# Kernel optimization log

Hardware: AMD Instinct MI355X
Metric: run time of the kernel (lower is better)

## Reference

```python
import jax, jax.numpy as jnp
import numpy as np

B, T, C, H, U = 16, 2048, 512, 4, 250
L, R = 1, 1              # l_order, r_order -> depthwise kernel size 3
K = L + R + 1
SMOOTH, NOISE = 1.0, 0.0  # smooth_factor, noise_threshold


def setup_inputs() -> dict:
    key = jax.random.key(0)
    k0, k1, k2, k3 = jax.random.split(key, 4)
    hidden = jax.random.normal(k0, (B, T, C), dtype=jnp.float32)
    mask = jnp.ones((B, 1, T), dtype=jnp.float32)
    target_label_length = jax.random.randint(k1, (B,), 0, U).astype(jnp.int32)
    # parameters
    conv_w = jax.random.normal(k2, (C, 1, K), dtype=jnp.float32) / np.sqrt(K)   # depthwise Conv1d weight [O, I/g=1, K]
    conv_b = jnp.zeros((C,), dtype=jnp.float32)
    lin_w = jax.random.normal(k3, (1, C), dtype=jnp.float32) / np.sqrt(C)       # cif_output Linear(idim, 1)
    lin_b = jnp.zeros((1,), dtype=jnp.float32)
    sigma = jnp.full((H,), 0.5, dtype=jnp.float32)
    sigma_bias = jnp.zeros((H,), dtype=jnp.float32)
    return {
        "hidden": hidden, "mask": mask, "target_label_length": target_label_length,
        "max_token": U, "conv_w": conv_w, "conv_b": conv_b,
        "lin_w": lin_w, "lin_b": lin_b, "sigma": sigma, "sigma_bias": sigma_bias,
    }


def reference(hidden, mask, target_label_length, max_token, conv_w, conv_b, lin_w, lin_b, sigma, sigma_bias):
    b, t, c = hidden.shape
    h = sigma.shape[0]
    # --- alpha prediction branch ---
    context = jnp.swapaxes(hidden, 1, 2)                       # [B, C, T]
    queries = jnp.pad(context, ((0, 0), (0, 0), (L, R)))       # ConstantPad1d((l, r), 0)
    memory = jax.lax.conv_general_dilated(
        queries, conv_w, window_strides=(1,), padding='VALID',
        feature_group_count=c, dimension_numbers=('NCH', 'OIH', 'NCH'))
    memory = memory + conv_b[None, :, None]
    out = jnp.swapaxes(memory + context, 1, 2)                 # [B, T, C]  (dropout = identity in eval)
    out = jax.nn.relu(out)
    out = out @ lin_w.T + lin_b                                # [B, T, 1]
    alphas = jax.nn.relu(jax.nn.sigmoid(out) * SMOOTH - NOISE)
    mask_bt1 = jnp.swapaxes(mask, -1, -2)                      # [B, T, 1]
    alphas = (alphas * mask_bt1)[..., 0]                       # [B, T]
    mask_bt = mask_bt1[..., 0]                                 # [B, T]
    # --- CIF scaling to target length ---
    target_length = target_label_length.astype(jnp.float32)   # [B]
    token_num = alphas.sum(-1)                                 # [B] (pre-scaling, as in torch)
    alphas = alphas * (target_length / token_num)[:, None]
    alignment = jnp.cumsum(alphas, axis=-1)                    # [B, T]
    # --- Gaussian soft-segment attention ---
    fire_positions = jnp.arange(max_token, dtype=alphas.dtype) + 0.5            # [U]
    dist = fire_positions[None, None, :, None] - alignment[:, None, None, :]    # [B, 1, U, T]
    scores = -(dist * sigma[None, :, None, None]) ** 2 + sigma_bias[None, :, None, None]  # [B, H, U, T]
    scores = jnp.where(mask_bt[:, None, None, :] > 0, scores, -jnp.inf)
    weights = jax.nn.softmax(scores, axis=-1)                  # [B, H, U, T]
    n_hidden = hidden.reshape(b, t, h, c // h).transpose(0, 2, 1, 3)            # [B, H, T, Dh]
    acoustic = jnp.einsum('bhut,bhtd->bhud', weights, n_hidden)                 # [B, H, U, Dh]
    acoustic_embeds = acoustic.transpose(0, 2, 1, 3).reshape(b, max_token, c)   # [B, U, C]
    return acoustic_embeds, token_num, alphas
```

## Files before the change

kernel.cpp:

```cpp
#include <hip/hip_runtime.h>

namespace {
constexpr int kB = 16, kT = 2048, kC = 512, kH = 4, kU = 250, kDH = 128;
constexpr int kDS = 4;
constexpr int kDW = 32;
constexpr int kPitch = 2056;
constexpr int kNB = kDS * kH * kB;
constexpr int kNS = 16;
}

typedef __attribute__((ext_vector_type(8))) short short8;
typedef __attribute__((ext_vector_type(4))) float float4v;

__device__ __forceinline__ short f2bf(float x) {
    union { float f; unsigned int u; } v; v.f = x;
    unsigned int r = (v.u + 0x7FFFu + ((v.u >> 16) & 1u)) >> 16;
    return (short)r;
}

__global__ __launch_bounds__(1024) void fused_pif(
    const float* __restrict__ hid, const float* __restrict__ mask,
    const int* __restrict__ target, const float* __restrict__ sigma,
    const float* __restrict__ conv_w, const float* __restrict__ conv_b,
    const float* __restrict__ lin_w, const float* __restrict__ lin_b,
    float* __restrict__ part, unsigned int* __restrict__ counter,
    float* __restrict__ out_ac, float* __restrict__ out_tok, float* __restrict__ out_alpha)
{
    __shared__ unsigned short bV[kDW * kPitch];
    __shared__ float al_s[kT];
    __shared__ float woff[16];
    __shared__ float s_tot;

    const int ds = blockIdx.x, h = blockIdx.y, b = blockIdx.z;
    const int tid = threadIdx.x;
    const int wave = tid >> 6, lane = tid & 63;
    const int dl = lane & 7;
    const int q  = lane >> 3;
    const int cbase = h * kDH + ds * kDW;
    const int c0g = cbase + dl * 4;
    const int slice = h * kDS + ds;

    float cw0[4], cw1[4], cw2[4], cb4[4], lw4[4];
    {
        float4 w0 = *(const float4*)(conv_w + c0g * 3);
        float4 w1 = *(const float4*)(conv_w + c0g * 3 + 4);
        float4 w2 = *(const float4*)(conv_w + c0g * 3 + 8);
        cw0[0] = w0.x; cw1[0] = w0.y; cw2[0] = w0.z;
        cw0[1] = w0.w; cw1[1] = w1.x; cw2[1] = w1.y;
        cw0[2] = w1.z; cw1[2] = w1.w; cw2[2] = w2.x;
        cw0[3] = w2.y; cw1[3] = w2.z; cw2[3] = w2.w;
        *(float4*)cb4 = *(const float4*)(conv_b + c0g);
        *(float4*)lw4 = *(const float4*)(lin_w + c0g);
    }
    float* pp = part + ((size_t)slice * kB + b) * kT;
    const float* hrow = hid + (size_t)b * kT * kC + c0g;
    const int wbase = wave * 128;

    float4 A0[4], A1[4], B0[4], B1[4];
    float4 h2, h1;
    h2.x = h2.y = h2.z = h2.w = 0.f;
    h1 = h2;
    if (q == 0 && wave > 0) {
        const float* s = hrow + (size_t)(wbase - 2) * kC;
        h2 = *(const float4*)s;
        h1 = *(const float4*)(s + kC);
    }
    #pragma unroll
    for (int k = 0; k < 4; k++) {
        const float* s = hrow + (size_t)(wbase + k * 16 + 2 * q) * kC;
        A0[k] = *(const float4*)s;
        A1[k] = *(const float4*)(s + kC);
    }
    float4 Lp0, Lp1;
    Lp0 = h2; Lp1 = h1;

    #define PROC(kk, Ax, Ay)  {                                                  \
        const int t0 = wbase + (kk) * 16 + 2 * q;                                \
        float pm2[4], pm1[4];                                                    \
        _Pragma("unroll")                                                        \
        for (int e = 0; e < 4; e++) {                                            \
            float c2, c1v;                                                       \
            if ((kk) == 0) { c2 = ((float*)&h2)[e]; c1v = ((float*)&h1)[e]; }    \
            else {                                                               \
                c2  = __shfl(((float*)&Lp0)[e], 56 + dl, 64);                    \
                c1v = __shfl(((float*)&Lp1)[e], 56 + dl, 64);                    \
            }                                                                    \
            float s2 = __shfl_up(((float*)&Ax)[e], 8, 64);                       \
            float s1 = __shfl_up(((float*)&Ay)[e], 8, 64);                       \
            pm2[e] = (q == 0) ? c2  : s2;                                        \
            pm1[e] = (q == 0) ? c1v : s1;                                        \
        }                                                                        \
        _Pragma("unroll")                                                        \
        for (int e = 0; e < 4; e++) {                                            \
            unsigned int lo = (unsigned int)(unsigned short)f2bf(((float*)&Ax)[e]); \
            unsigned int hi = (unsigned int)(unsigned short)f2bf(((float*)&Ay)[e]); \
            *(unsigned int*)&bV[(dl * 4 + e) * kPitch + t0] = lo | (hi << 16);   \
        }                                                                        \
        float s_m1 = 0.f, s_0 = 0.f;                                             \
        _Pragma("unroll")                                                        \
        for (int e = 0; e < 4; e++) {                                            \
            float x_m2 = pm2[e], x_m1 = pm1[e];                                  \
            float x0 = ((float*)&Ax)[e], x1 = ((float*)&Ay)[e];                  \
            float m_a = fmaf(cw0[e], x_m2, fmaf(cw1[e], x_m1, fmaf(cw2[e], x0, cb4[e]))); \
            float v_a = m_a + x_m1; v_a = v_a > 0.f ? v_a : 0.f;                 \
            s_m1 = fmaf(v_a, lw4[e], s_m1);                                      \
            float m_b = fmaf(cw0[e], x_m1, fmaf(cw1[e], x0, fmaf(cw2[e], x1, cb4[e]))); \
            float v_b = m_b + x0; v_b = v_b > 0.f ? v_b : 0.f;                   \
            s_0 = fmaf(v_b, lw4[e], s_0);                                        \
        }                                                                        \
        _Pragma("unroll")                                                        \
        for (int off = 1; off <= 4; off <<= 1) {                                 \
            s_m1 += __shfl_xor(s_m1, off, 64);                                   \
            s_0  += __shfl_xor(s_0, off, 64);                                    \
        }                                                                        \
        if (dl == 0) {                                                           \
            if (t0 > 0) __hip_atomic_store(pp + (t0 - 1), s_m1,                  \
                            __ATOMIC_RELAXED, __HIP_MEMORY_SCOPE_AGENT);         \
            __hip_atomic_store(pp + t0, s_0,                                     \
                            __ATOMIC_RELAXED, __HIP_MEMORY_SCOPE_AGENT);         \
        }                                                                        \
        Lp0 = Ax; Lp1 = Ay; }

    PROC(0, A0[0], A1[0])
    #pragma unroll
    for (int k = 0; k < 4; k++) {
        const float* s = hrow + (size_t)(wbase + 64 + k * 16 + 2 * q) * kC;
        B0[k] = *(const float4*)s;
        B1[k] = *(const float4*)(s + kC);
    }
    PROC(1, A0[1], A1[1])
    PROC(2, A0[2], A1[2])
    PROC(3, A0[3], A1[3])
    PROC(4, B0[0], B1[0])
    PROC(5, B0[1], B1[1])
    PROC(6, B0[2], B1[2])
    PROC(7, B0[3], B1[3])
    #undef PROC

    if (wave == 15 && q == 7) {
        float sacc = 0.f;
        #pragma unroll
        for (int e = 0; e < 4; e++) {
            float xm1 = ((float*)&Lp0)[e];
            float x0  = ((float*)&Lp1)[e];
            float m = fmaf(cw0[e], xm1, fmaf(cw1[e], x0, cb4[e]));
            float v = m + x0; v = v > 0.f ? v : 0.f;
            sacc = fmaf(v, lw4[e], sacc);
        }
        #pragma unroll
        for (int off = 1; off <= 4; off <<= 1) sacc += __shfl_xor(sacc, off, 64);
        if (dl == 0) __hip_atomic_store(pp + (kT - 1), sacc,
                         __ATOMIC_RELAXED, __HIP_MEMORY_SCOPE_AGENT);
    }

    __syncthreads();
    if (tid == 0) {
        __hip_atomic_fetch_add(counter, 1u, __ATOMIC_RELEASE, __HIP_MEMORY_SCOPE_AGENT);
        long long guard = 0;
        while (__hip_atomic_load(counter, __ATOMIC_RELAXED, __HIP_MEMORY_SCOPE_AGENT) < (unsigned)kNB) {
            __builtin_amdgcn_s_sleep(2);
            if (++guard > (3LL << 20)) break;
        }
    }
    __syncthreads();

    const int lm = lane & 15, quad = lane >> 4;
    const float sig = sigma[h];
    const float lb = lin_b[0];

    float l0 = 0.f, l1 = 0.f;
    #pragma unroll
    for (int s = 0; s < kNS; s++) {
        unsigned long long uv = __hip_atomic_load(
            (const unsigned long long*)(part + ((size_t)s * kB + b) * kT + 2 * tid),
            __ATOMIC_RELAXED, __HIP_MEMORY_SCOPE_AGENT);
        union { unsigned long long u; float2 f; } cv; cv.u = uv;
        l0 += cv.f.x; l1 += cv.f.y;
    }
    float2 mv = ((const float2*)(mask + (size_t)b * kT))[tid];
    float aw0 = (1.f / (1.f + expf(-(l0 + lb)))) * mv.x;
    float aw1 = (1.f / (1.f + expf(-(l1 + lb)))) * mv.y;

    const float p0 = aw0, p1v = aw0 + aw1;
    float sc = p1v;
    #pragma unroll
    for (int off = 1; off <= 32; off <<= 1) {
        float v = __shfl_up(sc, off, 64);
        sc = (lane >= off) ? sc + v : sc;
    }
    if (lane == 63) woff[wave] = sc;
    __syncthreads();
    if (tid == 0) {
        float run = 0.f;
        #pragma unroll
        for (int w = 0; w < 16; w++) { float x = woff[w]; woff[w] = run; run += x; }
        s_tot = run;
    }
    __syncthreads();
    const float tot = s_tot;
    const float scale = (tot != 0.f) ? ((float)target[b] / tot) : 0.f;
    const float basev = woff[wave] + (sc - p1v);
    {
        float c0 = (basev + p0) * scale;
        float c1 = (basev + p1v) * scale;
        float2 alv;
        alv.x = (mv.x > 0.f) ? c0 : 1.0e30f;
        alv.y = (mv.y > 0.f) ? c1 : 1.0e30f;
        ((float2*)al_s)[tid] = alv;
    }
    if (ds == 0 && h == 0) {
        if (tid == 0) out_tok[b] = tot;
        float2 oa; oa.x = aw0 * scale; oa.y = aw1 * scale;
        ((float2*)(out_alpha + (size_t)b * kT))[tid] = oa;
    }
    __syncthreads();

    const int u_base = wave * 16;
    const float du = (float)(u_base + lm) + 0.5f;
    const float dusig = du * sig;
    int pos = 0;
    #pragma unroll
    for (int stp = 1024; stp >= 1; stp >>= 1) {
        int np = pos + stp;
        pos = (al_s[np - 1] < du) ? np : pos;
    }
    float d1 = (pos < kT) ? al_s[pos] - du : 3.0e30f;
    float d0 = (pos > 0) ? du - al_s[pos - 1] : 3.0e30f;
    float dmin = fminf(d0, d1);
    float ms = fminf(dmin, 1.0e4f) * sig;
    const float mu_pos = ms * ms;

    float dmax_l = fminf(dmin, 1.0e4f);
    #pragma unroll
    for (int off = 8; off >= 1; off >>= 1) dmax_l = fmaxf(dmax_l, __shfl_xor(dmax_l, off, 64));
    const float c21 = (sig > 1e-3f) ? 21.0f / (sig * sig) : 9.0e60f;
    const float bound = sqrtf(fmaf(dmax_l, dmax_l, c21));
    const float lo_b = (float)u_base + 0.5f - bound;
    const float hi_b = (float)u_base + 15.5f + bound;
    int p_lo = 0, p_hi = 0;
    #pragma unroll
    for (int stp = 1024; stp >= 1; stp >>= 1) {
        int n1 = p_lo + stp; p_lo = (al_s[n1 - 1] < lo_b) ? n1 : p_lo;
        int n2 = p_hi + stp; p_hi = (al_s[n2 - 1] < hi_b) ? n2 : p_hi;
    }
    const int ks_lo = p_lo >> 5;
    const int ks_end = (p_hi + 31) >> 5;

    float4v acc0 = (float4v)(0.f), acc1 = (float4v)(0.f);
    float lsum = 0.f;

    for (int kg = ks_lo; kg < ks_end; kg++) {
        const int kb = kg * 32;
        float alv[8];
        *(float4*)&alv[0] = *(const float4*)&al_s[kb + quad * 8];
        *(float4*)&alv[4] = *(const float4*)&al_s[kb + quad * 8 + 4];

        short8 afrag;
        #pragma unroll
        for (int j = 0; j < 8; j++) {
            float d = fmaf(-alv[j], sig, dusig);
            float e = __expf(fmaf(-d, d, mu_pos));
            lsum += e;
            afrag[j] = f2bf(e);
        }
        short8 bf0 = *(const short8*)&bV[lm * kPitch + kb + quad * 8];
        short8 bf1 = *(const short8*)&bV[(16 + lm) * kPitch + kb + quad * 8];
        acc0 = __builtin_amdgcn_mfma_f32_16x16x32_bf16(afrag, bf0, acc0, 0, 0, 0);
        acc1 = __builtin_amdgcn_mfma_f32_16x16x32_bf16(afrag, bf1, acc1, 0, 0, 0);
    }

    float lv = lsum;
    lv += __shfl_xor(lv, 16, 64);
    lv += __shfl_xor(lv, 32, 64);
    #pragma unroll
    for (int r = 0; r < 4; r++) {
        const int ur = quad * 4 + r;
        float rl = __shfl(lv, ur, 64);
        float linv = (rl > 1e-30f) ? 1.f / rl : 0.f;
        const int u = u_base + ur;
        if (u < kU) {
            float* dst = out_ac + ((size_t)(b * kU + u)) * kC + h * kDH + ds * kDW + lm;
            dst[0]  = acc0[r] * linv;
            dst[16] = acc1[r] * linv;
        }
    }
}

extern "C" void kernel_launch(void* const* d_in, const int* in_sizes, int n_in,
                              void* d_out, int out_size, void* d_ws, size_t ws_size,
                              hipStream_t stream) {
    const float* hid    = (const float*)d_in[0];
    const float* mask   = (const float*)d_in[1];
    const int*   tgt    = (const int*)d_in[2];
    const float* conv_w = (const float*)d_in[4];
    const float* conv_b = (const float*)d_in[5];
    const float* lin_w  = (const float*)d_in[6];
    const float* lin_b  = (const float*)d_in[7];
    const float* sigma  = (const float*)d_in[8];

    unsigned int* counter = (unsigned int*)d_ws;
    float* part = (float*)((char*)d_ws + 256);

    float* out_ac    = (float*)d_out;
    float* out_tok   = out_ac + (size_t)kB * kU * kC;
    float* out_alpha = out_tok + kB;

    hipMemsetAsync(d_ws, 0, 256, stream);
    fused_pif<<<dim3(kDS, kH, kB), 1024, 0, stream>>>(
        hid, mask, tgt, sigma, conv_w, conv_b, lin_w, lin_b,
        part, counter, out_ac, out_tok, out_alpha);
}
```

Measured before the change: 147.4 us.

## Accumulate logits via atomic adds, use hardware bf16 pack and exp2 intrinsics

Per-slice logit partials are now staged in LDS and added with atomics into one shared per-batch buffer, replacing 16 separate partial rows that every block later had to read back and sum. The workspace memset grows to zero that buffer. The bf16 conversion uses the packed hardware convert instruction, and the Gaussian exponent uses a raw v_exp_f32 with sigma pre-scaled by sqrt(log2 e). Hidden-state loads become a rolling three-stage register prefetch instead of two large batches, which lowers register pressure. Float atomic ordering makes the sums nondeterministic, and the packed convert and raw exp may round slightly differently from the old code.

Result: no change. 145.0 us (-1.6%).

```diff
diff --git a/kernel.cpp b/kernel.cpp
--- a/kernel.cpp
+++ b/kernel.cpp
@@ -6,7 +6,6 @@
 constexpr int kDW = 32;
 constexpr int kPitch = 2056;
 constexpr int kNB = kDS * kH * kB;
-constexpr int kNS = 16;
 }
 
 typedef __attribute__((ext_vector_type(8))) short short8;
@@ -16,6 +15,16 @@
     union { float f; unsigned int u; } v; v.f = x;
     unsigned int r = (v.u + 0x7FFFu + ((v.u >> 16) & 1u)) >> 16;
     return (short)r;
+}
+__device__ __forceinline__ unsigned int pk_bf16(float lo, float hi) {
+    unsigned int r;
+    asm volatile("v_cvt_pk_bf16_f32 %0, %1, %2" : "=v"(r) : "v"(lo), "v"(hi));
+    return r;
+}
+__device__ __forceinline__ float exp2_fast(float x) {
+    float r;
+    asm volatile("v_exp_f32 %0, %1" : "=v"(r) : "v"(x));
+    return r;
 }
 
 __global__ __launch_bounds__(1024) void fused_pif(
@@ -38,7 +47,6 @@
     const int q  = lane >> 3;
     const int cbase = h * kDH + ds * kDW;
     const int c0g = cbase + dl * 4;
-    const int slice = h * kDS + ds;
 
     float cw0[4], cw1[4], cw2[4], cb4[4], lw4[4];
     {
@@ -52,11 +60,10 @@
         *(float4*)cb4 = *(const float4*)(conv_b + c0g);
         *(float4*)lw4 = *(const float4*)(lin_w + c0g);
     }
-    float* pp = part + ((size_t)slice * kB + b) * kT;
+    float* pacc = part + (size_t)b * kT;
     const float* hrow = hid + (size_t)b * kT * kC + c0g;
     const int wbase = wave * 128;
 
-    float4 A0[4], A1[4], B0[4], B1[4];
     float4 h2, h1;
     h2.x = h2.y = h2.z = h2.w = 0.f;
     h1 = h2;
@@ -65,12 +72,12 @@
         h2 = *(const float4*)s;
         h1 = *(const float4*)(s + kC);
     }
-    #pragma unroll
-    for (int k = 0; k < 4; k++) {
-        const float* s = hrow + (size_t)(wbase + k * 16 + 2 * q) * kC;
-        A0[k] = *(const float4*)s;
-        A1[k] = *(const float4*)(s + kC);
-    }
+    float4 xa0, xa1, xb0, xb1, xc0, xc1;
+    #define LOADP(X, Y, kk) { const float* s_ = hrow + (size_t)(wbase + (kk) * 16 + 2 * q) * kC; \
+                              X = *(const float4*)s_; Y = *(const float4*)(s_ + kC); }
+    LOADP(xa0, xa1, 0)
+    LOADP(xb0, xb1, 1)
+    LOADP(xc0, xc1, 2)
     float4 Lp0, Lp1;
     Lp0 = h2; Lp1 = h1;
 
@@ -92,9 +99,8 @@
         }                                                                        \
         _Pragma("unroll")                                                        \
         for (int e = 0; e < 4; e++) {                                            \
-            unsigned int lo = (unsigned int)(unsigned short)f2bf(((float*)&Ax)[e]); \
-            unsigned int hi = (unsigned int)(unsigned short)f2bf(((float*)&Ay)[e]); \
-            *(unsigned int*)&bV[(dl * 4 + e) * kPitch + t0] = lo | (hi << 16);   \
+            unsigned int w_ = pk_bf16(((float*)&Ax)[e], ((float*)&Ay)[e]);       \
+            *(unsigned int*)&bV[(dl * 4 + e) * kPitch + t0] = w_;                \
         }                                                                        \
         float s_m1 = 0.f, s_0 = 0.f;                                             \
         _Pragma("unroll")                                                        \
@@ -114,28 +120,21 @@
             s_0  += __shfl_xor(s_0, off, 64);                                    \
         }                                                                        \
         if (dl == 0) {                                                           \
-            if (t0 > 0) __hip_atomic_store(pp + (t0 - 1), s_m1,                  \
-                            __ATOMIC_RELAXED, __HIP_MEMORY_SCOPE_AGENT);         \
-            __hip_atomic_store(pp + t0, s_0,                                     \
-                            __ATOMIC_RELAXED, __HIP_MEMORY_SCOPE_AGENT);         \
+            if (t0 > 0) al_s[t0 - 1] = s_m1;                                     \
+            al_s[t0] = s_0;                                                      \
         }                                                                        \
         Lp0 = Ax; Lp1 = Ay; }
 
-    PROC(0, A0[0], A1[0])
-    #pragma unroll
-    for (int k = 0; k < 4; k++) {
-        const float* s = hrow + (size_t)(wbase + 64 + k * 16 + 2 * q) * kC;
-        B0[k] = *(const float4*)s;
-        B1[k] = *(const float4*)(s + kC);
-    }
-    PROC(1, A0[1], A1[1])
-    PROC(2, A0[2], A1[2])
-    PROC(3, A0[3], A1[3])
-    PROC(4, B0[0], B1[0])
-    PROC(5, B0[1], B1[1])
-    PROC(6, B0[2], B1[2])
-    PROC(7, B0[3], B1[3])
+    PROC(0, xa0, xa1) LOADP(xa0, xa1, 3)
+    PROC(1, xb0, xb1) LOADP(xb0, xb1, 4)
+    PROC(2, xc0, xc1) LOADP(xc0, xc1, 5)
+    PROC(3, xa0, xa1) LOADP(xa0, xa1, 6)
+    PROC(4, xb0, xb1) LOADP(xb0, xb1, 7)
+    PROC(5, xc0, xc1)
+    PROC(6, xa0, xa1)
+    PROC(7, xb0, xb1)
     #undef PROC
+    #undef LOADP
 
     if (wave == 15 && q == 7) {
         float sacc = 0.f;
@@ -149,8 +148,14 @@
         }
         #pragma unroll
         for (int off = 1; off <= 4; off <<= 1) sacc += __shfl_xor(sacc, off, 64);
-        if (dl == 0) __hip_atomic_store(pp + (kT - 1), sacc,
-                         __ATOMIC_RELAXED, __HIP_MEMORY_SCOPE_AGENT);
+        if (dl == 0) al_s[kT - 1] = sacc;
+    }
+    __syncthreads();
+
+    {
+        float2 pv = ((const float2*)al_s)[tid];
+        unsafeAtomicAdd(pacc + 2 * tid, pv.x);
+        unsafeAtomicAdd(pacc + 2 * tid + 1, pv.y);
     }
 
     __syncthreads();
@@ -166,20 +171,15 @@
 
     const int lm = lane & 15, quad = lane >> 4;
     const float sig = sigma[h];
+    const float sigL = sig * 1.2011224f;
     const float lb = lin_b[0];
 
-    float l0 = 0.f, l1 = 0.f;
-    #pragma unroll
-    for (int s = 0; s < kNS; s++) {
-        unsigned long long uv = __hip_atomic_load(
-            (const unsigned long long*)(part + ((size_t)s * kB + b) * kT + 2 * tid),
-            __ATOMIC_RELAXED, __HIP_MEMORY_SCOPE_AGENT);
-        union { unsigned long long u; float2 f; } cv; cv.u = uv;
-        l0 += cv.f.x; l1 += cv.f.y;
-    }
+    union { unsigned long long u; float2 f; } cv;
+    cv.u = __hip_atomic_load((const unsigned long long*)(pacc + 2 * tid),
+                             __ATOMIC_RELAXED, __HIP_MEMORY_SCOPE_AGENT);
     float2 mv = ((const float2*)(mask + (size_t)b * kT))[tid];
-    float aw0 = (1.f / (1.f + expf(-(l0 + lb)))) * mv.x;
-    float aw1 = (1.f / (1.f + expf(-(l1 + lb)))) * mv.y;
+    float aw0 = (1.f / (1.f + expf(-(cv.f.x + lb)))) * mv.x;
+    float aw1 = (1.f / (1.f + expf(-(cv.f.y + lb)))) * mv.y;
 
     const float p0 = aw0, p1v = aw0 + aw1;
     float sc = p1v;
@@ -217,7 +217,7 @@
 
     const int u_base = wave * 16;
     const float du = (float)(u_base + lm) + 0.5f;
-    const float dusig = du * sig;
+    const float duL = du * sigL;
     int pos = 0;
     #pragma unroll
     for (int stp = 1024; stp >= 1; stp >>= 1) {
@@ -227,7 +227,7 @@
     float d1 = (pos < kT) ? al_s[pos] - du : 3.0e30f;
     float d0 = (pos > 0) ? du - al_s[pos - 1] : 3.0e30f;
     float dmin = fminf(d0, d1);
-    float ms = fminf(dmin, 1.0e4f) * sig;
+    float ms = fminf(dmin, 1.0e4f) * sigL;
     const float mu_pos = ms * ms;
 
     float dmax_l = fminf(dmin, 1.0e4f);
@@ -255,18 +255,23 @@
         *(float4*)&alv[0] = *(const float4*)&al_s[kb + quad * 8];
         *(float4*)&alv[4] = *(const float4*)&al_s[kb + quad * 8 + 4];
 
-        short8 afrag;
+        float ev[8];
         #pragma unroll
         for (int j = 0; j < 8; j++) {
-            float d = fmaf(-alv[j], sig, dusig);
-            float e = __expf(fmaf(-d, d, mu_pos));
+            float d = fmaf(-alv[j], sigL, duL);
+            float e = exp2_fast(fmaf(-d, d, mu_pos));
             lsum += e;
-            afrag[j] = f2bf(e);
+            ev[j] = e;
         }
+        union { short8 s; unsigned int w[4]; } af;
+        af.w[0] = pk_bf16(ev[0], ev[1]);
+        af.w[1] = pk_bf16(ev[2], ev[3]);
+        af.w[2] = pk_bf16(ev[4], ev[5]);
+        af.w[3] = pk_bf16(ev[6], ev[7]);
         short8 bf0 = *(const short8*)&bV[lm * kPitch + kb + quad * 8];
         short8 bf1 = *(const short8*)&bV[(16 + lm) * kPitch + kb + quad * 8];
-        acc0 = __builtin_amdgcn_mfma_f32_16x16x32_bf16(afrag, bf0, acc0, 0, 0, 0);
-        acc1 = __builtin_amdgcn_mfma_f32_16x16x32_bf16(afrag, bf1, acc1, 0, 0, 0);
+        acc0 = __builtin_amdgcn_mfma_f32_16x16x32_bf16(af.s, bf0, acc0, 0, 0, 0);
+        acc1 = __builtin_amdgcn_mfma_f32_16x16x32_bf16(af.s, bf1, acc1, 0, 0, 0);
     }
 
     float lv = lsum;
@@ -305,7 +310,7 @@
     float* out_tok   = out_ac + (size_t)kB * kU * kC;
     float* out_alpha = out_tok + kB;
 
-    hipMemsetAsync(d_ws, 0, 256, stream);
+    hipMemsetAsync(d_ws, 0, 256 + (size_t)kB * kT * 4, stream);
     fused_pif<<<dim3(kDS, kH, kB), 1024, 0, stream>>>(
         hid, mask, tgt, sigma, conv_w, conv_b, lin_w, lin_b,
         part, counter, out_ac, out_tok, out_alpha);
```
